# Kernel optimization log

Measured on AMD Instinct MI355X. Metric: run time of the kernel, lower is better.

## Reference

```python
import jax, jax.numpy as jnp
import numpy as np

N = 100000   # nodes
E = 1600000  # edges per meta-path graph
D_IN = 256
H = 4        # num_heads
F = 32       # out_feats per head
D_HID = H * F  # 128
D_SEM = 128  # semantic attention hidden dim
C = 8        # output classes
NEG_SLOPE = 0.2


def setup_inputs() -> dict:
    key = jax.random.key(0)
    ks = jax.random.split(key, 24)
    inp = {
        "x": jax.random.normal(ks[0], (N, D_IN), dtype=jnp.float32),
        "src0": jax.random.randint(ks[1], (E,), 0, N),
        "dst0": jax.random.randint(ks[2], (E,), 0, N),
        "ew0": jax.random.uniform(ks[3], (E,), dtype=jnp.float32),
        "src1": jax.random.randint(ks[4], (E,), 0, N),
        "dst1": jax.random.randint(ks[5], (E,), 0, N),
        "ew1": jax.random.uniform(ks[6], (E,), dtype=jnp.float32),
    }
    s_in = 1.0 / np.sqrt(D_IN)
    s_f = 1.0 / np.sqrt(F)
    s_h = 1.0 / np.sqrt(D_HID)
    s_s = 1.0 / np.sqrt(D_SEM)
    # GAT params for meta-path 0 and 1 (tuple feat -> separate fc_src/fc_dst)
    inp["Wsrc0"] = jax.random.normal(ks[7], (D_IN, D_HID), dtype=jnp.float32) * s_in
    inp["Wdst0"] = jax.random.normal(ks[8], (D_IN, D_HID), dtype=jnp.float32) * s_in
    inp["al0"] = jax.random.normal(ks[9], (H, F), dtype=jnp.float32) * s_f
    inp["ar0"] = jax.random.normal(ks[10], (H, F), dtype=jnp.float32) * s_f
    inp["b0"] = jnp.zeros((D_HID,), dtype=jnp.float32)
    inp["Wsrc1"] = jax.random.normal(ks[11], (D_IN, D_HID), dtype=jnp.float32) * s_in
    inp["Wdst1"] = jax.random.normal(ks[12], (D_IN, D_HID), dtype=jnp.float32) * s_in
    inp["al1"] = jax.random.normal(ks[13], (H, F), dtype=jnp.float32) * s_f
    inp["ar1"] = jax.random.normal(ks[14], (H, F), dtype=jnp.float32) * s_f
    inp["b1"] = jnp.zeros((D_HID,), dtype=jnp.float32)
    # Semantic attention: Linear(D_HID->128) -> tanh -> Linear(128->1, no bias)
    inp["Wp1"] = jax.random.normal(ks[15], (D_HID, D_SEM), dtype=jnp.float32) * s_h
    inp["bp1"] = jnp.zeros((D_SEM,), dtype=jnp.float32)
    inp["Wp2"] = jax.random.normal(ks[16], (D_SEM, 1), dtype=jnp.float32) * s_s
    # Prediction head
    inp["Wo"] = jax.random.normal(ks[17], (D_HID, C), dtype=jnp.float32) * s_h
    inp["bo"] = jnp.zeros((C,), dtype=jnp.float32)
    return inp


def gat_conv(x, Wsrc, Wdst, al, ar, b, src, dst, ew):
    # feat_src/feat_dst: [N, H, F]
    fs = (x @ Wsrc).reshape(N, H, F)
    fd = (x @ Wdst).reshape(N, H, F)
    el = jnp.einsum('nhf,hf->nh', fs, al)  # [N, H]
    er = jnp.einsum('nhf,hf->nh', fd, ar)  # [N, H]
    e = jax.nn.leaky_relu(el[src] + er[dst], negative_slope=NEG_SLOPE)  # [E, H]
    a = jax.nn.sigmoid(e) * ew[:, None]  # [E, H]  (sigmoid attention * edge_weight)
    m = fs[src] * a[:, :, None]  # [E, H, F]
    out = jax.ops.segment_sum(m, dst, num_segments=N)  # [N, H, F]
    out = out + b.reshape(1, H, F)
    return jax.nn.elu(out).reshape(N, H * F)


def semantic_attention(z, Wp1, bp1, Wp2):
    # z: [N, P, D_HID]
    w = jnp.tanh(z @ Wp1 + bp1) @ Wp2  # [N, P, 1]
    w = w.mean(axis=0)                  # [P, 1]
    beta = jax.nn.softmax(w, axis=0)    # softmax over meta-paths
    return (beta[None] * z).sum(axis=1)  # [N, D_HID]


def reference(x, src0, dst0, ew0, src1, dst1, ew1,
              Wsrc0, Wdst0, al0, ar0, b0,
              Wsrc1, Wdst1, al1, ar1, b1,
              Wp1, bp1, Wp2, Wo, bo):
    z0 = gat_conv(x, Wsrc0, Wdst0, al0, ar0, b0, src0, dst0, ew0)
    z1 = gat_conv(x, Wsrc1, Wdst1, al1, ar1, b1, src1, dst1, ew1)
    z = jnp.stack([z0, z1], axis=1)  # [N, 2, H*F]
    h = semantic_attention(z, Wp1, bp1, Wp2)  # [N, H*F]
    return h @ Wo + bo  # [N, C]
```

## Files before the change

kernel.cpp:

```cpp
#include <hip/hip_runtime.h>
#include <hip/hip_fp16.h>
#include <math.h>

#define N_NODES 100000
#define N_EDGES 1600000
#define D_IN    256
#define D_HID   128
#define NH      4
#define NF      32
#define D_SEM   128
#define NC      8
#define NEG_SLOPE 0.2f
#define BUCKET  64
#define BIN_SHIFT 9
#define BINS    196
#define BIN_CAP 9216
#define CHUNK   8192

typedef _Float16 half8 __attribute__((ext_vector_type(8)));
typedef float    floatx4 __attribute__((ext_vector_type(4)));

__global__ void prep_fold(const float* __restrict__ Ws0, const float* __restrict__ al0,
                          const float* __restrict__ Wd0, const float* __restrict__ ar0,
                          const float* __restrict__ Ws1, const float* __restrict__ al1,
                          const float* __restrict__ Wd1, const float* __restrict__ ar1,
                          float* __restrict__ WF) {
    int d = threadIdx.x;
    for (int p = 0; p < 2; ++p) {
        const float* Ws = p ? Ws1 : Ws0;
        const float* al = p ? al1 : al0;
        const float* Wd = p ? Wd1 : Wd0;
        const float* ar = p ? ar1 : ar0;
        for (int h = 0; h < NH; ++h) {
            float se = 0.f, sr = 0.f;
            for (int f = 0; f < NF; ++f) {
                se = fmaf(Ws[d*D_HID + h*NF + f], al[h*NF + f], se);
                sr = fmaf(Wd[d*D_HID + h*NF + f], ar[h*NF + f], sr);
            }
            WF[d*16 + p*8 + h]     = se;
            WF[d*16 + p*8 + 4 + h] = sr;
        }
    }
}

__global__ __launch_bounds__(256) void prep_tr(const float* __restrict__ Ws0,
                                               const float* __restrict__ Ws1,
                                               const float* __restrict__ Wp1,
                                               __half* __restrict__ WT0,
                                               __half* __restrict__ WT1,
                                               __half* __restrict__ WP1T) {
    int g = blockIdx.x * 256 + threadIdx.x;
    if (g < 32768) {
        int c = g >> 8, k = g & 255;
        WT0[g] = __float2half_rn(Ws0[k*D_HID + c]);
    } else if (g < 65536) {
        int g2 = g - 32768;
        int c = g2 >> 8, k = g2 & 255;
        WT1[g2] = __float2half_rn(Ws1[k*D_HID + c]);
    } else {
        int g2 = g - 65536;
        int c = g2 >> 7, k = g2 & 127;
        WP1T[g2] = __float2half_rn(Wp1[k*D_SEM + c]);
    }
}

__global__ __launch_bounds__(256) void er_el_kernel(const float* __restrict__ x,
                                                    const float* __restrict__ WF,
                                                    float* __restrict__ eler,
                                                    __half* __restrict__ XH) {
    __shared__ float xs[16][260];
    __shared__ float wfs[4096];
    int tid = threadIdx.x;
    #pragma unroll
    for (int i = 0; i < 16; ++i) wfs[tid + i*256] = WF[tid + i*256];
    int n0 = blockIdx.x * 16;
    #pragma unroll
    for (int i = 0; i < 4; ++i) {
        int id = tid + i*256;
        int r = id >> 6, c = (id & 63) << 2;
        *(float4*)&xs[r][c] = *(const float4*)&x[(size_t)(n0 + r)*D_IN + c];
    }
    __syncthreads();
    int node = tid >> 4, c = tid & 15;
    float s = 0.f;
    #pragma unroll 8
    for (int k = 0; k < 256; ++k) s = fmaf(xs[node][k], wfs[k*16 + c], s);
    int p = c >> 3, e = (c >> 2) & 1, h = c & 3;
    eler[(p*2 + e)*400000 + (n0 + node)*4 + h] = s;

    #pragma unroll
    for (int i = 0; i < 4; ++i) {
        int id = tid + i*256;
        int r = id >> 6, c4 = (id & 63) << 2;
        float4 v = *(const float4*)&xs[r][c4];
        __half2 h0 = __floats2half2_rn(v.x, v.y);
        __half2 h1 = __floats2half2_rn(v.z, v.w);
        uint2 pk; pk.x = *(unsigned*)&h0; pk.y = *(unsigned*)&h1;
        *(uint2*)&XH[(size_t)(n0 + r)*D_IN + c4] = pk;
    }
}

__global__ __launch_bounds__(256) void gemm_fs_mfma(const __half* __restrict__ XH,
                                                    const __half* __restrict__ WT,
                                                    __half* __restrict__ FS) {
    __shared__ unsigned short xs[64][64];
    __shared__ unsigned short ws[128][64];
    int tid = threadIdx.x;
    int row0 = blockIdx.x * 64;
    int wid = tid >> 6, lane = tid & 63;
    int wm = wid >> 1, wn = wid & 1;
    int lr = lane & 15, lk = lane >> 4;

    floatx4 acc[2][4];
    #pragma unroll
    for (int m = 0; m < 2; ++m)
        #pragma unroll
        for (int n = 0; n < 4; ++n) acc[m][n] = (floatx4){0.f, 0.f, 0.f, 0.f};

    for (int k0 = 0; k0 < D_IN; k0 += 64) {
        #pragma unroll
        for (int i = 0; i < 2; ++i) {
            int id = tid + i*256;
            int r = id >> 3, c8 = (id & 7) << 3;
            int grow = row0 + r;
            uint4 pk = make_uint4(0u, 0u, 0u, 0u);
            if (grow < N_NODES) pk = *(const uint4*)&XH[(size_t)grow*D_IN + k0 + c8];
            int cc = (((c8 >> 3) ^ (r & 7)) << 3);
            *(uint4*)&xs[r][cc] = pk;
        }
        #pragma unroll
        for (int i = 0; i < 8; ++i) {
            int id = tid + i*256;
            int col = id >> 4, c4 = (id & 15) << 2;
            uint2 pk = *(const uint2*)&WT[col*256 + k0 + c4];
            int cc = (((c4 >> 3) ^ (col & 7)) << 3) + (c4 & 7);
            *(uint2*)&ws[col][cc] = pk;
        }
        __syncthreads();
        #pragma unroll
        for (int kk = 0; kk < 2; ++kk) {
            int ksub = kk*4 + lk;
            half8 a[2], b[4];
            #pragma unroll
            for (int m = 0; m < 2; ++m) {
                int r = wm*32 + m*16 + lr;
                a[m] = *(half8*)&xs[r][((ksub ^ (r & 7)) << 3)];
            }
            #pragma unroll
            for (int n = 0; n < 4; ++n) {
                int c = wn*64 + n*16 + lr;
                b[n] = *(half8*)&ws[c][((ksub ^ (c & 7)) << 3)];
            }
            #pragma unroll
            for (int m = 0; m < 2; ++m)
                #pragma unroll
                for (int n = 0; n < 4; ++n)
                    acc[m][n] = __builtin_amdgcn_mfma_f32_16x16x32_f16(a[m], b[n], acc[m][n], 0, 0, 0);
        }
        __syncthreads();
    }

    unsigned short* outs = &ws[0][0];
    #pragma unroll
    for (int m = 0; m < 2; ++m)
        #pragma unroll
        for (int n = 0; n < 4; ++n) {
            int col = wn*64 + n*16 + lr;
            #pragma unroll
            for (int r4 = 0; r4 < 4; ++r4) {
                int rr = wm*32 + m*16 + lk*4 + r4;
                __half hv = __float2half_rn(acc[m][n][r4]);
                outs[rr*128 + col] = *(unsigned short*)&hv;
            }
        }
    __syncthreads();
    #pragma unroll
    for (int i = 0; i < 8; ++i) {
        int id = tid + i*256;
        int r = id >> 5, c4 = (id & 31) << 2;
        int grow = row0 + r;
        if (grow < N_NODES)
            *(uint2*)&FS[(size_t)grow*D_HID + c4] = *(uint2*)&outs[r*128 + c4];
    }
}

__global__ __launch_bounds__(1024) void bin_kernel(const int* __restrict__ src,
                                                   const int* __restrict__ dst,
                                                   const float* __restrict__ ew,
                                                   int* __restrict__ gcur,
                                                   uint2* __restrict__ binned) {
    __shared__ uint2 stage[CHUNK];
    __shared__ unsigned char binof[CHUNK];
    __shared__ int bcnt[256], boff[256], gbase[256], brun[256];
    int tid = threadIdx.x;
    int c0 = blockIdx.x * CHUNK;
    int C = N_EDGES - c0; if (C > CHUNK) C = CHUNK;
    if (C <= 0) return;

    if (tid < 256) bcnt[tid] = 0;
    __syncthreads();
    for (int j = tid; j < C; j += 1024)
        atomicAdd(&bcnt[dst[c0 + j] >> BIN_SHIFT], 1);
    __syncthreads();

    int v = (tid < 256) ? bcnt[tid] : 0;
    if (tid < 256) boff[tid] = v;
    __syncthreads();
    for (int o = 1; o < 256; o <<= 1) {
        int u = (tid < 256 && tid >= o) ? boff[tid - o] : 0;
        __syncthreads();
        if (tid < 256) boff[tid] += u;
        __syncthreads();
    }
    if (tid < 256) {
        boff[tid] -= v;
        brun[tid] = 0;
        if (tid < BINS) gbase[tid] = v ? atomicAdd(&gcur[tid], v) : 0;
    }
    __syncthreads();

    for (int j = tid; j < C; j += 1024) {
        int e = c0 + j;
        int d = dst[e];
        int b = d >> BIN_SHIFT;
        unsigned q = (unsigned)(ew[e] * 32767.f + 0.5f);
        int p = atomicAdd(&brun[b], 1);
        int sl = boff[b] + p;
        stage[sl] = make_uint2(((unsigned)src[e] << 15) | q, (unsigned)d);
        binof[sl] = (unsigned char)b;
    }
    __syncthreads();

    for (int j = tid; j < C; j += 1024) {
        int b = binof[j];
        int off = gbase[b] + (j - boff[b]);
        if (off < BIN_CAP) binned[b * BIN_CAP + off] = stage[j];
    }
}

__global__ __launch_bounds__(1024) void bucket_kernel(const int* __restrict__ gcur,
                                                      const uint2* __restrict__ binned,
                                                      int* __restrict__ cnt,
                                                      unsigned* __restrict__ edg) {
    __shared__ unsigned buck[512 * BUCKET];
    __shared__ int lcnt[512];
    int tid = threadIdx.x;
    int b = blockIdx.x;
    int n0 = b << BIN_SHIFT;
    if (tid < 512) lcnt[tid] = 0;
    __syncthreads();

    int cE = gcur[b]; if (cE > BIN_CAP) cE = BIN_CAP;
    for (int j = tid; j < cE; j += 1024) {
        uint2 r = binned[b * BIN_CAP + j];
        int dl = (int)r.y - n0;
        int p = atomicAdd(&lcnt[dl], 1);
        if (p < BUCKET) buck[(dl << 6) + p] = r.x;
    }
    __syncthreads();

    const uint4* b4 = (const uint4*)buck;
    uint4* e4 = (uint4*)edg;
    for (int i = tid; i < 512 * BUCKET / 4; i += 1024) {
        int node = n0 + (i >> 4);
        int used = lcnt[i >> 4];
        if (node < N_NODES && ((i & 15) << 2) < used)
            e4[((size_t)node << 4) + (i & 15)] = b4[i];
    }
    if (tid < 512) {
        int node = n0 + tid;
        if (node < N_NODES) cnt[node] = lcnt[tid] < BUCKET ? lcnt[tid] : BUCKET;
    }
}

__global__ __launch_bounds__(256) void agg_kernel(const __half* __restrict__ FS,
                                                  const float* __restrict__ el,
                                                  const float* __restrict__ er,
                                                  const int* __restrict__ cnt,
                                                  const unsigned* __restrict__ edg,
                                                  const float* __restrict__ bias,
                                                  __half* __restrict__ zh) {
    int wv = (blockIdx.x * 256 + threadIdx.x) >> 6;
    int lane = threadIdx.x & 63;
    if (wv >= N_NODES) return;
    int q  = lane >> 4;
    int ql = lane & 15;
    int hh = lane & 3;
    float erh = er[wv*4 + hh];
    int cn = cnt[wv];
    if (cn > BUCKET) cn = BUCKET;
    int beg = wv << 6;
    const __half* fsq = FS + (ql << 3);

    float4 a0 = make_float4(0.f,0.f,0.f,0.f);
    float4 a1 = make_float4(0.f,0.f,0.f,0.f);

    int nIt = (cn + 15) >> 4;
    for (int it = 0; it < nIt; ++it) {
        int jb = it << 4;
        int sl = jb + (lane >> 2);
        int slc = sl < cn ? sl : cn - 1;
        unsigned w = edg[beg + slc];
        int s = (int)(w >> 15);
        float a = (float)(w & 32767u) * (1.f / 32767.f);
        float v = el[s*4 + hh] + erh;
        v = v > 0.f ? v : NEG_SLOPE * v;
        a = a * __builtin_amdgcn_rcpf(1.f + __expf(-v));
        a = sl < cn ? a : 0.f;
        #pragma unroll
        for (int u = 0; u < 4; ++u) {
            int e = (u << 2) + q;
            int su = jb + e;
            int ssrc = __shfl(s, e << 2);
            uint4 raw = make_uint4(0u, 0u, 0u, 0u);
            if (su < cn) raw = *(const uint4*)&fsq[(size_t)ssrc * D_HID];
            float av = __shfl(a, (e << 2) | (ql >> 2));
            float2 f0 = __half22float2(*(__half2*)&raw.x);
            float2 f1 = __half22float2(*(__half2*)&raw.y);
            float2 f2 = __half22float2(*(__half2*)&raw.z);
            float2 f3 = __half22float2(*(__half2*)&raw.w);
            a0.x = fmaf(f0.x, av, a0.x); a0.y = fmaf(f0.y, av, a0.y);
            a0.z = fmaf(f1.x, av, a0.z); a0.w = fmaf(f1.y, av, a0.w);
            a1.x = fmaf(f2.x, av, a1.x); a1.y = fmaf(f2.y, av, a1.y);
            a1.z = fmaf(f3.x, av, a1.z); a1.w = fmaf(f3.y, av, a1.w);
        }
    }

    #pragma unroll
    for (int o = 16; o < 64; o <<= 1) {
        a0.x += __shfl_xor(a0.x, o); a0.y += __shfl_xor(a0.y, o);
        a0.z += __shfl_xor(a0.z, o); a0.w += __shfl_xor(a0.w, o);
        a1.x += __shfl_xor(a1.x, o); a1.y += __shfl_xor(a1.y, o);
        a1.z += __shfl_xor(a1.z, o); a1.w += __shfl_xor(a1.w, o);
    }

    if (q < 2) {
        int c = (ql << 3) + (q << 2);
        float4 r = q ? a1 : a0;
        float4 bv = *(const float4*)&bias[c];
        r.x += bv.x; r.y += bv.y; r.z += bv.z; r.w += bv.w;
        r.x = r.x > 0.f ? r.x : expm1f(r.x);
        r.y = r.y > 0.f ? r.y : expm1f(r.y);
        r.z = r.z > 0.f ? r.z : expm1f(r.z);
        r.w = r.w > 0.f ? r.w : expm1f(r.w);
        __half2 h0 = __floats2half2_rn(r.x, r.y);
        __half2 h1 = __floats2half2_rn(r.z, r.w);
        uint2 pk; pk.x = *(unsigned*)&h0; pk.y = *(unsigned*)&h1;
        *(uint2*)&zh[(size_t)wv*D_HID + c] = pk;
    }
}

__global__ __launch_bounds__(256) void sem_mfma(const __half* __restrict__ zh0,
                                                const __half* __restrict__ zh1,
                                                const __half* __restrict__ WP1T,
                                                const float* __restrict__ bp1,
                                                const float* __restrict__ Wp2,
                                                float* __restrict__ wsum) {
    __shared__ unsigned short zs[64][128];
    __shared__ unsigned short ps[128][128];
    __shared__ float red[4];
    const __half* z = blockIdx.y ? zh1 : zh0;
    int tid = threadIdx.x;
    int row0 = blockIdx.x * 64;
    int wid = tid >> 6, lane = tid & 63;
    int wm = wid >> 1, wn = wid & 1;
    int lr = lane & 15, lk = lane >> 4;

    #pragma unroll
    for (int i = 0; i < 4; ++i) {
        int id = tid + i*256;
        int r = id >> 4, ch = id & 15;
        int grow = row0 + r;
        uint4 pk = make_uint4(0u, 0u, 0u, 0u);
        if (grow < N_NODES) pk = *(const uint4*)&z[(size_t)grow*D_HID + (ch << 3)];
        *(uint4*)&zs[r][((ch ^ (r & 7)) << 3)] = pk;
    }
    #pragma unroll
    for (int i = 0; i < 16; ++i) {
        int id = tid + i*256;
        int c = id >> 5, k4 = (id & 31) << 2;
        uint2 pk = *(const uint2*)&WP1T[c*128 + k4];
        int cc = (((k4 >> 3) ^ (c & 7)) << 3) + (k4 & 7);
        *(uint2*)&ps[c][cc] = pk;
    }
    __syncthreads();

    floatx4 acc[2][4];
    #pragma unroll
    for (int m = 0; m < 2; ++m)
        #pragma unroll
        for (int n = 0; n < 4; ++n) acc[m][n] = (floatx4){0.f, 0.f, 0.f, 0.f};

    #pragma unroll
    for (int kk = 0; kk < 4; ++kk) {
        int ksub = kk*4 + lk;
        half8 a[2], b[4];
        #pragma unroll
        for (int m = 0; m < 2; ++m) {
            int r = wm*32 + m*16 + lr;
            a[m] = *(half8*)&zs[r][((ksub ^ (r & 7)) << 3)];
        }
        #pragma unroll
        for (int n = 0; n < 4; ++n) {
            int c = wn*64 + n*16 + lr;
            b[n] = *(half8*)&ps[c][((ksub ^ (c & 7)) << 3)];
        }
        #pragma unroll
        for (int m = 0; m < 2; ++m)
            #pragma unroll
            for (int n = 0; n < 4; ++n)
                acc[m][n] = __builtin_amdgcn_mfma_f32_16x16x32_f16(a[m], b[n], acc[m][n], 0, 0, 0);
    }

    float s = 0.f;
    #pragma unroll
    for (int m = 0; m < 2; ++m)
        #pragma unroll
        for (int n = 0; n < 4; ++n) {
            int col = wn*64 + n*16 + lr;
            float bp = bp1[col];
            float w2 = Wp2[col];
            #pragma unroll
            for (int r4 = 0; r4 < 4; ++r4) {
                int grow = row0 + wm*32 + m*16 + lk*4 + r4;
                if (grow < N_NODES) {
                    float v = acc[m][n][r4] + bp;
                    float t = 1.f - 2.f / (__expf(2.f*v) + 1.f);
                    s = fmaf(t, w2, s);
                }
            }
        }
    #pragma unroll
    for (int o = 1; o < 64; o <<= 1) s += __shfl_xor(s, o);
    if (lane == 0) red[wid] = s;
    __syncthreads();
    if (tid == 0) atomicAdd(&wsum[blockIdx.y], red[0] + red[1] + red[2] + red[3]);
}

__global__ __launch_bounds__(256) void final_kernel(const __half* __restrict__ zh0,
                                                    const __half* __restrict__ zh1,
                                                    const float* __restrict__ Wo,
                                                    const float* __restrict__ bo,
                                                    const float* __restrict__ wsum,
                                                    float* __restrict__ out) {
    __shared__ float z0s[32][132];
    __shared__ float z1s[32][132];
    __shared__ float wos[128*8];
    __shared__ float bos[8];
    int tid = threadIdx.x;
    int n0 = blockIdx.x * 32;
    #pragma unroll
    for (int i = 0; i < 4; ++i) wos[tid + i*256] = Wo[tid + i*256];
    if (tid < 8) bos[tid] = bo[tid];
    #pragma unroll
    for (int i = 0; i < 2; ++i) {
        int id = tid + i*256;
        int r = id >> 4, c8 = (id & 15) << 3;
        uint4 p0 = *(const uint4*)&zh0[(size_t)(n0 + r)*D_HID + c8];
        uint4 p1 = *(const uint4*)&zh1[(size_t)(n0 + r)*D_HID + c8];
        float2 q0 = __half22float2(*(__half2*)&p0.x);
        float2 q1 = __half22float2(*(__half2*)&p0.y);
        float2 q2 = __half22float2(*(__half2*)&p0.z);
        float2 q3 = __half22float2(*(__half2*)&p0.w);
        *(float4*)&z0s[r][c8]     = make_float4(q0.x, q0.y, q1.x, q1.y);
        *(float4*)&z0s[r][c8 + 4] = make_float4(q2.x, q2.y, q3.x, q3.y);
        q0 = __half22float2(*(__half2*)&p1.x);
        q1 = __half22float2(*(__half2*)&p1.y);
        q2 = __half22float2(*(__half2*)&p1.z);
        q3 = __half22float2(*(__half2*)&p1.w);
        *(float4*)&z1s[r][c8]     = make_float4(q0.x, q0.y, q1.x, q1.y);
        *(float4*)&z1s[r][c8 + 4] = make_float4(q2.x, q2.y, q3.x, q3.y);
    }
    __syncthreads();

    float w0 = wsum[0] * (1.f / N_NODES), w1 = wsum[1] * (1.f / N_NODES);
    float m = fmaxf(w0, w1);
    float e0 = __expf(w0 - m), e1 = __expf(w1 - m);
    float b0 = e0 / (e0 + e1), b1 = 1.f - b0;

    int node = tid >> 3, c = tid & 7;
    float s = bos[c];
    #pragma unroll 8
    for (int k = 0; k < 128; ++k) {
        float hk = b0 * z0s[node][k] + b1 * z1s[node][k];
        s = fmaf(hk, wos[k*8 + c], s);
    }
    out[(n0 + node)*NC + c] = s;
}

extern "C" void kernel_launch(void* const* d_in, const int* in_sizes, int n_in,
                              void* d_out, int out_size, void* d_ws, size_t ws_size,
                              hipStream_t stream) {
    const float* x     = (const float*)d_in[0];
    const int*   src0  = (const int*)  d_in[1];
    const int*   dst0  = (const int*)  d_in[2];
    const float* ew0   = (const float*)d_in[3];
    const int*   src1  = (const int*)  d_in[4];
    const int*   dst1  = (const int*)  d_in[5];
    const float* ew1   = (const float*)d_in[6];
    const float* Wsrc0 = (const float*)d_in[7];
    const float* Wdst0 = (const float*)d_in[8];
    const float* al0   = (const float*)d_in[9];
    const float* ar0   = (const float*)d_in[10];
    const float* b0    = (const float*)d_in[11];
    const float* Wsrc1 = (const float*)d_in[12];
    const float* Wdst1 = (const float*)d_in[13];
    const float* al1   = (const float*)d_in[14];
    const float* ar1   = (const float*)d_in[15];
    const float* b1    = (const float*)d_in[16];
    const float* Wp1   = (const float*)d_in[17];
    const float* bp1   = (const float*)d_in[18];
    const float* Wp2   = (const float*)d_in[19];
    const float* Wo    = (const float*)d_in[20];
    const float* bo    = (const float*)d_in[21];
    float* out = (float*)d_out;

    float*    ws     = (float*)d_ws;
    __half*   FS     = (__half*)ws;
    __half*   ZH0    = (__half*)(ws + 6400000);
    __half*   ZH1    = (__half*)(ws + 12800000);
    __half*   XH     = (__half*)(ws + 19200000);
    float*    ELER   = ws + 32000000;
    float*    WF     = ELER + 1600000;
    float*    WSUM   = WF + 4096;
    __half*   WT0    = (__half*)(WSUM + 8);
    __half*   WT1    = (__half*)((float*)WT0 + 16384);
    __half*   WP1T   = (__half*)((float*)WT1 + 16384);
    int*      CNT0   = (int*)((float*)WP1T + 8192);
    int*      CNT1   = CNT0  + 100000;
    int*      GCUR0  = CNT1  + 100000;
    int*      GCUR1  = GCUR0 + 256;
    unsigned* EDG    = (unsigned*)(GCUR1 + 256);
    uint2*    BINNED = (uint2*)(EDG + 6400000);

    hipMemsetAsync(GCUR0, 0, sizeof(int)*512, stream);
    hipMemsetAsync(WSUM, 0, sizeof(float)*4, stream);

    prep_fold<<<1, 256, 0, stream>>>(Wsrc0, al0, Wdst0, ar0, Wsrc1, al1, Wdst1, ar1, WF);
    prep_tr<<<320, 256, 0, stream>>>(Wsrc0, Wsrc1, Wp1, WT0, WT1, WP1T);
    er_el_kernel<<<N_NODES/16, 256, 0, stream>>>(x, WF, ELER, XH);

    bin_kernel<<<BINS, 1024, 0, stream>>>(src0, dst0, ew0, GCUR0, BINNED);
    bucket_kernel<<<BINS, 1024, 0, stream>>>(GCUR0, BINNED, CNT0, EDG);
    gemm_fs_mfma<<<(N_NODES + 63)/64, 256, 0, stream>>>(XH, WT0, FS);
    agg_kernel<<<(N_NODES*64)/256, 256, 0, stream>>>(FS, ELER, ELER + 400000, CNT0, EDG, b0, ZH0);

    bin_kernel<<<BINS, 1024, 0, stream>>>(src1, dst1, ew1, GCUR1, BINNED);
    bucket_kernel<<<BINS, 1024, 0, stream>>>(GCUR1, BINNED, CNT1, EDG);
    gemm_fs_mfma<<<(N_NODES + 63)/64, 256, 0, stream>>>(XH, WT1, FS);
    agg_kernel<<<(N_NODES*64)/256, 256, 0, stream>>>(FS, ELER + 800000, ELER + 1200000, CNT1, EDG, b1, ZH1);

    dim3 semgrid((N_NODES + 63)/64, 2);
    sem_mfma<<<semgrid, 256, 0, stream>>>(ZH0, ZH1, WP1T, bp1, Wp2, WSUM);
    final_kernel<<<N_NODES/32, 256, 0, stream>>>(ZH0, ZH1, Wo, bo, WSUM, out);
}
```

Measured before the change: 599.8 us.

## Halve bin width to double bin/bucket blocks and front-load edge loads in aggregation

Bins now cover 256 destination nodes instead of 512, so the bin and bucket kernels each launch about twice as many blocks and use less shared memory per block, giving more parallelism across CUs. The aggregation kernel now loads all four 16-edge groups of edge records, el values (as float4) and attention coefficients up front before the gather loop, exposing more memory-level parallelism than the per-iteration dependent loads. The cost is more registers per thread and a longer bin-offset scan.

```diff
diff --git a/kernel.cpp b/kernel.cpp
--- a/kernel.cpp
+++ b/kernel.cpp
@@ -12,10 +12,10 @@
 #define NC      8
 #define NEG_SLOPE 0.2f
 #define BUCKET  64
-#define BIN_SHIFT 9
-#define BINS    196
-#define BIN_CAP 9216
-#define CHUNK   8192
+#define BIN_SHIFT 8
+#define BINS    391
+#define BIN_CAP 4608
+#define CHUNK   4096
 
 typedef _Float16 half8 __attribute__((ext_vector_type(8)));
 typedef float    floatx4 __attribute__((ext_vector_type(4)));
@@ -190,29 +190,29 @@
                                                    int* __restrict__ gcur,
                                                    uint2* __restrict__ binned) {
     __shared__ uint2 stage[CHUNK];
-    __shared__ unsigned char binof[CHUNK];
-    __shared__ int bcnt[256], boff[256], gbase[256], brun[256];
+    __shared__ unsigned short binof[CHUNK];
+    __shared__ int bcnt[512], boff[512], gbase[512], brun[512];
     int tid = threadIdx.x;
     int c0 = blockIdx.x * CHUNK;
     int C = N_EDGES - c0; if (C > CHUNK) C = CHUNK;
     if (C <= 0) return;
 
-    if (tid < 256) bcnt[tid] = 0;
+    if (tid < 512) bcnt[tid] = 0;
     __syncthreads();
     for (int j = tid; j < C; j += 1024)
         atomicAdd(&bcnt[dst[c0 + j] >> BIN_SHIFT], 1);
     __syncthreads();
 
-    int v = (tid < 256) ? bcnt[tid] : 0;
-    if (tid < 256) boff[tid] = v;
-    __syncthreads();
-    for (int o = 1; o < 256; o <<= 1) {
-        int u = (tid < 256 && tid >= o) ? boff[tid - o] : 0;
+    int v = (tid < 512) ? bcnt[tid] : 0;
+    if (tid < 512) boff[tid] = v;
+    __syncthreads();
+    for (int o = 1; o < 512; o <<= 1) {
+        int u = (tid < 512 && tid >= o) ? boff[tid - o] : 0;
         __syncthreads();
-        if (tid < 256) boff[tid] += u;
+        if (tid < 512) boff[tid] += u;
         __syncthreads();
     }
-    if (tid < 256) {
+    if (tid < 512) {
         boff[tid] -= v;
         brun[tid] = 0;
         if (tid < BINS) gbase[tid] = v ? atomicAdd(&gcur[tid], v) : 0;
@@ -227,7 +227,7 @@
         int p = atomicAdd(&brun[b], 1);
         int sl = boff[b] + p;
         stage[sl] = make_uint2(((unsigned)src[e] << 15) | q, (unsigned)d);
-        binof[sl] = (unsigned char)b;
+        binof[sl] = (unsigned short)b;
     }
     __syncthreads();
 
@@ -242,12 +242,12 @@
                                                       const uint2* __restrict__ binned,
                                                       int* __restrict__ cnt,
                                                       unsigned* __restrict__ edg) {
-    __shared__ unsigned buck[512 * BUCKET];
-    __shared__ int lcnt[512];
+    __shared__ unsigned buck[256 * BUCKET];
+    __shared__ int lcnt[256];
     int tid = threadIdx.x;
     int b = blockIdx.x;
     int n0 = b << BIN_SHIFT;
-    if (tid < 512) lcnt[tid] = 0;
+    if (tid < 256) lcnt[tid] = 0;
     __syncthreads();
 
     int cE = gcur[b]; if (cE > BIN_CAP) cE = BIN_CAP;
@@ -261,16 +261,27 @@
 
     const uint4* b4 = (const uint4*)buck;
     uint4* e4 = (uint4*)edg;
-    for (int i = tid; i < 512 * BUCKET / 4; i += 1024) {
+    for (int i = tid; i < 256 * BUCKET / 4; i += 1024) {
         int node = n0 + (i >> 4);
         int used = lcnt[i >> 4];
         if (node < N_NODES && ((i & 15) << 2) < used)
             e4[((size_t)node << 4) + (i & 15)] = b4[i];
     }
-    if (tid < 512) {
+    if (tid < 256) {
         int node = n0 + tid;
         if (node < N_NODES) cnt[node] = lcnt[tid] < BUCKET ? lcnt[tid] : BUCKET;
     }
+}
+
+__device__ __forceinline__ float sel4(float4 v, int h) {
+    float ab = (h & 1) ? v.y : v.x;
+    float cd = (h & 1) ? v.w : v.z;
+    return (h & 2) ? cd : ab;
+}
+__device__ __forceinline__ float coef_of(unsigned w, float v) {
+    float a = (float)(w & 32767u) * (1.f / 32767.f);
+    v = v > 0.f ? v : NEG_SLOPE * v;
+    return a * __builtin_amdgcn_rcpf(1.f + __expf(-v));
 }
 
 __global__ __launch_bounds__(256) void agg_kernel(const __half* __restrict__ FS,
@@ -283,48 +294,61 @@
     int wv = (blockIdx.x * 256 + threadIdx.x) >> 6;
     int lane = threadIdx.x & 63;
     if (wv >= N_NODES) return;
-    int q  = lane >> 4;
-    int ql = lane & 15;
-    int hh = lane & 3;
-    float erh = er[wv*4 + hh];
+    int q   = lane >> 4;
+    int ql  = lane & 15;
+    int hh  = lane & 3;
+    int eL  = lane >> 2;
     int cn = cnt[wv];
     if (cn > BUCKET) cn = BUCKET;
     int beg = wv << 6;
     const __half* fsq = FS + (ql << 3);
 
+    unsigned w0 = 0, w1 = 0, w2 = 0, w3 = 0;
+    if (eL      < cn) w0 = edg[beg + eL];
+    if (eL + 16 < cn) w1 = edg[beg + 16 + eL];
+    if (eL + 32 < cn) w2 = edg[beg + 32 + eL];
+    if (eL + 48 < cn) w3 = edg[beg + 48 + eL];
+    int s0v = (int)(w0 >> 15), s1v = (int)(w1 >> 15);
+    int s2v = (int)(w2 >> 15), s3v = (int)(w3 >> 15);
+    float4 el0 = *(const float4*)&el[s0v*4];
+    float4 el1 = *(const float4*)&el[s1v*4];
+    float4 el2 = *(const float4*)&el[s2v*4];
+    float4 el3 = *(const float4*)&el[s3v*4];
+    float erh = sel4(*(const float4*)&er[wv*4], hh);
+    float c0v = (eL      < cn) ? coef_of(w0, sel4(el0, hh) + erh) : 0.f;
+    float c1v = (eL + 16 < cn) ? coef_of(w1, sel4(el1, hh) + erh) : 0.f;
+    float c2v = (eL + 32 < cn) ? coef_of(w2, sel4(el2, hh) + erh) : 0.f;
+    float c3v = (eL + 48 < cn) ? coef_of(w3, sel4(el3, hh) + erh) : 0.f;
+
     float4 a0 = make_float4(0.f,0.f,0.f,0.f);
     float4 a1 = make_float4(0.f,0.f,0.f,0.f);
-
-    int nIt = (cn + 15) >> 4;
-    for (int it = 0; it < nIt; ++it) {
-        int jb = it << 4;
-        int sl = jb + (lane >> 2);
-        int slc = sl < cn ? sl : cn - 1;
-        unsigned w = edg[beg + slc];
-        int s = (int)(w >> 15);
-        float a = (float)(w & 32767u) * (1.f / 32767.f);
-        float v = el[s*4 + hh] + erh;
-        v = v > 0.f ? v : NEG_SLOPE * v;
-        a = a * __builtin_amdgcn_rcpf(1.f + __expf(-v));
-        a = sl < cn ? a : 0.f;
-        #pragma unroll
-        for (int u = 0; u < 4; ++u) {
-            int e = (u << 2) + q;
-            int su = jb + e;
-            int ssrc = __shfl(s, e << 2);
-            uint4 raw = make_uint4(0u, 0u, 0u, 0u);
-            if (su < cn) raw = *(const uint4*)&fsq[(size_t)ssrc * D_HID];
-            float av = __shfl(a, (e << 2) | (ql >> 2));
-            float2 f0 = __half22float2(*(__half2*)&raw.x);
-            float2 f1 = __half22float2(*(__half2*)&raw.y);
-            float2 f2 = __half22float2(*(__half2*)&raw.z);
-            float2 f3 = __half22float2(*(__half2*)&raw.w);
-            a0.x = fmaf(f0.x, av, a0.x); a0.y = fmaf(f0.y, av, a0.y);
-            a0.z = fmaf(f1.x, av, a0.z); a0.w = fmaf(f1.y, av, a0.w);
-            a1.x = fmaf(f2.x, av, a1.x); a1.y = fmaf(f2.y, av, a1.y);
-            a1.z = fmaf(f3.x, av, a1.z); a1.w = fmaf(f3.y, av, a1.w);
-        }
-    }
+    int qsh = q << 2, hsel = ql >> 2;
+
+#define AGG_PHASE(SP, CP, BASE)                                               \
+    if ((BASE) < cn) {                                                        \
+        _Pragma("unroll")                                                     \
+        for (int u = 0; u < 4; ++u) {                                         \
+            int lsrc = (u << 4) | qsh;                                        \
+            int ssrc = __shfl(SP, lsrc);                                      \
+            float av = __shfl(CP, lsrc | hsel);                               \
+            uint4 raw = make_uint4(0u,0u,0u,0u);                              \
+            if ((BASE) + (u << 2) + q < cn)                                   \
+                raw = *(const uint4*)&fsq[(size_t)ssrc * D_HID];              \
+            float2 f0 = __half22float2(*(__half2*)&raw.x);                    \
+            float2 f1 = __half22float2(*(__half2*)&raw.y);                    \
+            float2 f2 = __half22float2(*(__half2*)&raw.z);                    \
+            float2 f3 = __half22float2(*(__half2*)&raw.w);                    \
+            a0.x = fmaf(f0.x, av, a0.x); a0.y = fmaf(f0.y, av, a0.y);         \
+            a0.z = fmaf(f1.x, av, a0.z); a0.w = fmaf(f1.y, av, a0.w);         \
+            a1.x = fmaf(f2.x, av, a1.x); a1.y = fmaf(f2.y, av, a1.y);         \
+            a1.z = fmaf(f3.x, av, a1.z); a1.w = fmaf(f3.y, av, a1.w);         \
+        }                                                                     \
+    }
+    AGG_PHASE(s0v, c0v, 0)
+    AGG_PHASE(s1v, c1v, 16)
+    AGG_PHASE(s2v, c2v, 32)
+    AGG_PHASE(s3v, c3v, 48)
+#undef AGG_PHASE
 
     #pragma unroll
     for (int o = 16; o < 64; o <<= 1) {
@@ -529,23 +553,23 @@
     int*      CNT0   = (int*)((float*)WP1T + 8192);
     int*      CNT1   = CNT0  + 100000;
     int*      GCUR0  = CNT1  + 100000;
-    int*      GCUR1  = GCUR0 + 256;
-    unsigned* EDG    = (unsigned*)(GCUR1 + 256);
+    int*      GCUR1  = GCUR0 + 512;
+    unsigned* EDG    = (unsigned*)(GCUR1 + 512);
     uint2*    BINNED = (uint2*)(EDG + 6400000);
 
-    hipMemsetAsync(GCUR0, 0, sizeof(int)*512, stream);
+    hipMemsetAsync(GCUR0, 0, sizeof(int)*1024, stream);
     hipMemsetAsync(WSUM, 0, sizeof(float)*4, stream);
 
     prep_fold<<<1, 256, 0, stream>>>(Wsrc0, al0, Wdst0, ar0, Wsrc1, al1, Wdst1, ar1, WF);
     prep_tr<<<320, 256, 0, stream>>>(Wsrc0, Wsrc1, Wp1, WT0, WT1, WP1T);
     er_el_kernel<<<N_NODES/16, 256, 0, stream>>>(x, WF, ELER, XH);
 
-    bin_kernel<<<BINS, 1024, 0, stream>>>(src0, dst0, ew0, GCUR0, BINNED);
+    bin_kernel<<<(N_EDGES + CHUNK - 1)/CHUNK, 1024, 0, stream>>>(src0, dst0, ew0, GCUR0, BINNED);
     bucket_kernel<<<BINS, 1024, 0, stream>>>(GCUR0, BINNED, CNT0, EDG);
     gemm_fs_mfma<<<(N_NODES + 63)/64, 256, 0, stream>>>(XH, WT0, FS);
     agg_kernel<<<(N_NODES*64)/256, 256, 0, stream>>>(FS, ELER, ELER + 400000, CNT0, EDG, b0, ZH0);
 
-    bin_kernel<<<BINS, 1024, 0, stream>>>(src1, dst1, ew1, GCUR1, BINNED);
+    bin_kernel<<<(N_EDGES + CHUNK - 1)/CHUNK, 1024, 0, stream>>>(src1, dst1, ew1, GCUR1, BINNED);
     bucket_kernel<<<BINS, 1024, 0, stream>>>(GCUR1, BINNED, CNT1, EDG);
     gemm_fs_mfma<<<(N_NODES + 63)/64, 256, 0, stream>>>(XH, WT1, FS);
     agg_kernel<<<(N_NODES*64)/256, 256, 0, stream>>>(FS, ELER + 800000, ELER + 1200000, CNT1, EDG, b1, ZH1);
```

Result: no change. 610.7 us (+1.8%).

## Batch bin/bucket kernels across meta-paths and split bucket bins in half

Applied to the files above, without the earlier changes.

Bin and bucket kernels for both meta-path graphs are launched once each with a second grid dimension, using separate per-path edge buffers when the workspace is large enough. The bucket kernel now handles half a bin (256 nodes) per block, halving its shared memory and quadrupling block count. This aims to fill the GPU better and raise occupancy. In exchange, each bin's edge list is read twice and more workspace is needed, with a fallback to sequential launches otherwise.

```diff
diff --git a/kernel.cpp b/kernel.cpp
--- a/kernel.cpp
+++ b/kernel.cpp
@@ -19,6 +19,20 @@
 
 typedef _Float16 half8 __attribute__((ext_vector_type(8)));
 typedef float    floatx4 __attribute__((ext_vector_type(4)));
+
+struct BinArgs {
+    const int*   src[2];
+    const int*   dst[2];
+    const float* ew[2];
+    int*         gcur[2];
+    uint2*       binned[2];
+};
+struct BucketArgs {
+    const int*   gcur[2];
+    const uint2* binned[2];
+    int*         cnt[2];
+    unsigned*    edg[2];
+};
 
 __global__ void prep_fold(const float* __restrict__ Ws0, const float* __restrict__ al0,
                           const float* __restrict__ Wd0, const float* __restrict__ ar0,
@@ -184,14 +198,17 @@
     }
 }
 
-__global__ __launch_bounds__(1024) void bin_kernel(const int* __restrict__ src,
-                                                   const int* __restrict__ dst,
-                                                   const float* __restrict__ ew,
-                                                   int* __restrict__ gcur,
-                                                   uint2* __restrict__ binned) {
+__global__ __launch_bounds__(1024) void bin_kernel(BinArgs A) {
     __shared__ uint2 stage[CHUNK];
     __shared__ unsigned char binof[CHUNK];
     __shared__ int bcnt[256], boff[256], gbase[256], brun[256];
+    int P = blockIdx.y;
+    const int*   src = A.src[P];
+    const int*   dst = A.dst[P];
+    const float* ew  = A.ew[P];
+    int*         gcur = A.gcur[P];
+    uint2*       binned = A.binned[P];
+
     int tid = threadIdx.x;
     int c0 = blockIdx.x * CHUNK;
     int C = N_EDGES - c0; if (C > CHUNK) C = CHUNK;
@@ -238,36 +255,44 @@
     }
 }
 
-__global__ __launch_bounds__(1024) void bucket_kernel(const int* __restrict__ gcur,
-                                                      const uint2* __restrict__ binned,
-                                                      int* __restrict__ cnt,
-                                                      unsigned* __restrict__ edg) {
-    __shared__ unsigned buck[512 * BUCKET];
-    __shared__ int lcnt[512];
+__global__ __launch_bounds__(1024) void bucket_kernel(BucketArgs A) {
+    __shared__ unsigned buck[256 * BUCKET];
+    __shared__ int lcnt[256];
+    int P = blockIdx.y;
+    const int*   gcur   = A.gcur[P];
+    const uint2* binned = A.binned[P];
+    int*         cnt    = A.cnt[P];
+    unsigned*    edg    = A.edg[P];
+
     int tid = threadIdx.x;
-    int b = blockIdx.x;
-    int n0 = b << BIN_SHIFT;
-    if (tid < 512) lcnt[tid] = 0;
+    int nb = blockIdx.x;
+    int b  = nb >> 1;
+    int n0 = nb << 8;
+    int lo = (nb & 1) << 8;
+    if (tid < 256) lcnt[tid] = 0;
     __syncthreads();
 
     int cE = gcur[b]; if (cE > BIN_CAP) cE = BIN_CAP;
+    int bn0 = b << BIN_SHIFT;
     for (int j = tid; j < cE; j += 1024) {
         uint2 r = binned[b * BIN_CAP + j];
-        int dl = (int)r.y - n0;
-        int p = atomicAdd(&lcnt[dl], 1);
-        if (p < BUCKET) buck[(dl << 6) + p] = r.x;
+        int w = ((int)r.y - bn0) - lo;
+        if ((unsigned)w < 256u) {
+            int p = atomicAdd(&lcnt[w], 1);
+            if (p < BUCKET) buck[(w << 6) + p] = r.x;
+        }
     }
     __syncthreads();
 
     const uint4* b4 = (const uint4*)buck;
     uint4* e4 = (uint4*)edg;
-    for (int i = tid; i < 512 * BUCKET / 4; i += 1024) {
+    for (int i = tid; i < 256 * BUCKET / 4; i += 1024) {
         int node = n0 + (i >> 4);
         int used = lcnt[i >> 4];
         if (node < N_NODES && ((i & 15) << 2) < used)
             e4[((size_t)node << 4) + (i & 15)] = b4[i];
     }
-    if (tid < 512) {
+    if (tid < 256) {
         int node = n0 + tid;
         if (node < N_NODES) cnt[node] = lcnt[tid] < BUCKET ? lcnt[tid] : BUCKET;
     }
@@ -530,8 +555,14 @@
     int*      CNT1   = CNT0  + 100000;
     int*      GCUR0  = CNT1  + 100000;
     int*      GCUR1  = GCUR0 + 256;
-    unsigned* EDG    = (unsigned*)(GCUR1 + 256);
-    uint2*    BINNED = (uint2*)(EDG + 6400000);
+    unsigned* EDG0   = (unsigned*)(GCUR1 + 256);
+    uint2*    BINNED0= (uint2*)(EDG0 + 6400000);
+    float*    endser = (float*)BINNED0 + 2*(size_t)BINS*BIN_CAP;
+    unsigned* EDG1   = (unsigned*)endser;
+    uint2*    BINNED1= (uint2*)(EDG1 + 6400000);
+    size_t fused_bytes = (size_t)((float*)BINNED1 + 2*(size_t)BINS*BIN_CAP - ws) * 4;
+    bool fused = ws_size >= fused_bytes;
+    if (!fused) { EDG1 = EDG0; BINNED1 = BINNED0; }
 
     hipMemsetAsync(GCUR0, 0, sizeof(int)*512, stream);
     hipMemsetAsync(WSUM, 0, sizeof(float)*4, stream);
@@ -540,15 +571,36 @@
     prep_tr<<<320, 256, 0, stream>>>(Wsrc0, Wsrc1, Wp1, WT0, WT1, WP1T);
     er_el_kernel<<<N_NODES/16, 256, 0, stream>>>(x, WF, ELER, XH);
 
-    bin_kernel<<<BINS, 1024, 0, stream>>>(src0, dst0, ew0, GCUR0, BINNED);
-    bucket_kernel<<<BINS, 1024, 0, stream>>>(GCUR0, BINNED, CNT0, EDG);
-    gemm_fs_mfma<<<(N_NODES + 63)/64, 256, 0, stream>>>(XH, WT0, FS);
-    agg_kernel<<<(N_NODES*64)/256, 256, 0, stream>>>(FS, ELER, ELER + 400000, CNT0, EDG, b0, ZH0);
-
-    bin_kernel<<<BINS, 1024, 0, stream>>>(src1, dst1, ew1, GCUR1, BINNED);
-    bucket_kernel<<<BINS, 1024, 0, stream>>>(GCUR1, BINNED, CNT1, EDG);
-    gemm_fs_mfma<<<(N_NODES + 63)/64, 256, 0, stream>>>(XH, WT1, FS);
-    agg_kernel<<<(N_NODES*64)/256, 256, 0, stream>>>(FS, ELER + 800000, ELER + 1200000, CNT1, EDG, b1, ZH1);
+    int nchunks = (N_EDGES + CHUNK - 1) / CHUNK;
+    if (fused) {
+        BinArgs ba = {{src0, src1}, {dst0, dst1}, {ew0, ew1},
+                      {GCUR0, GCUR1}, {BINNED0, BINNED1}};
+        bin_kernel<<<dim3(nchunks, 2), 1024, 0, stream>>>(ba);
+        BucketArgs ka = {{GCUR0, GCUR1}, {BINNED0, BINNED1},
+                         {CNT0, CNT1}, {EDG0, EDG1}};
+        bucket_kernel<<<dim3(2*BINS, 2), 1024, 0, stream>>>(ka);
+        gemm_fs_mfma<<<(N_NODES + 63)/64, 256, 0, stream>>>(XH, WT0, FS);
+        agg_kernel<<<(N_NODES*64)/256, 256, 0, stream>>>(FS, ELER, ELER + 400000, CNT0, EDG0, b0, ZH0);
+        gemm_fs_mfma<<<(N_NODES + 63)/64, 256, 0, stream>>>(XH, WT1, FS);
+        agg_kernel<<<(N_NODES*64)/256, 256, 0, stream>>>(FS, ELER + 800000, ELER + 1200000, CNT1, EDG1, b1, ZH1);
+    } else {
+        BinArgs ba0 = {{src0, src0}, {dst0, dst0}, {ew0, ew0},
+                       {GCUR0, GCUR0}, {BINNED0, BINNED0}};
+        BucketArgs ka0 = {{GCUR0, GCUR0}, {BINNED0, BINNED0},
+                          {CNT0, CNT0}, {EDG0, EDG0}};
+        bin_kernel<<<dim3(nchunks, 1), 1024, 0, stream>>>(ba0);
+        bucket_kernel<<<dim3(2*BINS, 1), 1024, 0, stream>>>(ka0);
+        gemm_fs_mfma<<<(N_NODES + 63)/64, 256, 0, stream>>>(XH, WT0, FS);
+        agg_kernel<<<(N_NODES*64)/256, 256, 0, stream>>>(FS, ELER, ELER + 400000, CNT0, EDG0, b0, ZH0);
+        BinArgs ba1 = {{src1, src1}, {dst1, dst1}, {ew1, ew1},
+                       {GCUR1, GCUR1}, {BINNED0, BINNED0}};
+        BucketArgs ka1 = {{GCUR1, GCUR1}, {BINNED0, BINNED0},
+                          {CNT1, CNT1}, {EDG0, EDG0}};
+        bin_kernel<<<dim3(nchunks, 1), 1024, 0, stream>>>(ba1);
+        bucket_kernel<<<dim3(2*BINS, 1), 1024, 0, stream>>>(ka1);
+        gemm_fs_mfma<<<(N_NODES + 63)/64, 256, 0, stream>>>(XH, WT1, FS);
+        agg_kernel<<<(N_NODES*64)/256, 256, 0, stream>>>(FS, ELER + 800000, ELER + 1200000, CNT1, EDG0, b1, ZH1);
+    }
 
     dim3 semgrid((N_NODES + 63)/64, 2);
     sem_mfma<<<semgrid, 256, 0, stream>>>(ZH0, ZH1, WP1T, bp1, Wp2, WSUM);
```

After: 580.1 us. -3.3%, faster.
